# Kernel optimization log

Hardware: AMD Instinct MI355X
Metric: run time of the kernel (lower is better)

Reference implementation:

```python
import jax, jax.numpy as jnp
import numpy as np

B, IN_CH, HID, OUT_CH, GH, GW = 16, 64, 128, 64, 64, 64


def grid_edges(h, w):
    # torch_geometric.utils.grid: 8-neighborhood + self-loop, edge = (node, node+offset)
    idx = np.arange(h * w).reshape(h, w)
    rows, cols = [], []
    for dr in (-1, 0, 1):
        for dc in (-1, 0, 1):
            node = idx[max(0, -dr):h - max(0, dr), max(0, -dc):w - max(0, dc)]
            nb = idx[max(0, dr):h + min(0, dr) or None, max(0, dc):w + min(0, dc) or None]
            rows.append(node.ravel())
            cols.append(nb.ravel())
    return np.stack([np.concatenate(rows), np.concatenate(cols)])


def setup_inputs() -> dict:
    key = jax.random.key(0)
    ks = jax.random.split(key, 32)
    def rn(i, shape, scale=0.05):
        return jax.random.normal(ks[i], shape, dtype=jnp.float32) * scale
    e = grid_edges(GH, GW)                                   # (2, E)
    offs = (np.arange(B) * (GH * GW)).reshape(B, 1, 1)
    ei = (e[None] + offs).transpose(1, 0, 2).reshape(2, -1)  # (2, B*E) batched offsets
    return {
        "x": rn(0, (B, IN_CH, GH, GW), 1.0),
        "cW1": rn(1, (HID, IN_CH, 3, 3)), "cb1": rn(2, (HID,)),
        "cW2": rn(3, (IN_CH, HID, 3, 3)), "cb2": rn(4, (IN_CH,)),
        "q1W": rn(5, (HID, IN_CH)), "q1b": rn(6, (HID,)),
        "k1W": rn(7, (HID, IN_CH)), "k1b": rn(8, (HID,)),
        "v1W": rn(9, (HID, IN_CH)), "v1b": rn(10, (HID,)),
        "s1W": rn(11, (HID, IN_CH)), "s1b": rn(12, (HID,)),
        "q2W": rn(13, (IN_CH, HID)), "q2b": rn(14, (IN_CH,)),
        "k2W": rn(15, (IN_CH, HID)), "k2b": rn(16, (IN_CH,)),
        "v2W": rn(17, (IN_CH, HID)), "v2b": rn(18, (IN_CH,)),
        "s2W": rn(19, (IN_CH, HID)), "s2b": rn(20, (IN_CH,)),
        "fW1": rn(21, (HID, 2 * IN_CH, 3, 3)), "fb1": rn(22, (HID,)),
        "fW2": rn(23, (OUT_CH, HID, 3, 3)), "fb2": rn(24, (OUT_CH,)),
        "edge_index": jnp.asarray(ei, dtype=jnp.int32),
    }


def gelu(x):
    return jax.nn.gelu(x, approximate=False)


def sn_conv(x, W, b):
    # spectral_norm: power iteration on (O, I*k*k) matrix; u,v detached, grad through sigma
    O = W.shape[0]
    Wm = W.reshape(O, -1)
    u = jnp.ones((O,), W.dtype) / jnp.sqrt(jnp.asarray(O, W.dtype))
    for _ in range(3):
        v = Wm.T @ u
        v = v / (jnp.linalg.norm(v) + 1e-12)
        u = Wm @ v
        u = u / (jnp.linalg.norm(u) + 1e-12)
    u = jax.lax.stop_gradient(u)
    v = jax.lax.stop_gradient(v)
    sigma = u @ (Wm @ v)
    Wn = W / sigma
    xp = jnp.pad(x, ((0, 0), (0, 0), (1, 1), (1, 1)), mode='edge')  # replicate padding
    y = jax.lax.conv_general_dilated(xp, Wn, (1, 1), 'VALID',
                                     dimension_numbers=('NCHW', 'OIHW', 'NCHW'))
    return y + b[None, :, None, None]


def tconv(x, src, dst, N, heads, qW, qb, kW, kb, vW, vb, sW, sb):
    # PyG TransformerConv (concat=True, root_weight=True, no edge features)
    d = qW.shape[0] // heads
    q = (x @ qW.T + qb)[dst].reshape(-1, heads, d)
    k = (x @ kW.T + kb)[src].reshape(-1, heads, d)
    v = (x @ vW.T + vb)[src].reshape(-1, heads, d)
    alpha = (q * k).sum(-1) / jnp.sqrt(jnp.asarray(d, x.dtype))      # (E, heads)
    m = jax.ops.segment_max(alpha, dst, num_segments=N)               # scatter-softmax
    a = jnp.exp(alpha - m[dst])
    s = jax.ops.segment_sum(a, dst, num_segments=N)
    a = a / (s[dst] + 1e-16)
    out = jax.ops.segment_sum(a[:, :, None] * v, dst, num_segments=N)  # (N, heads, d)
    return out.reshape(N, heads * d) + x @ sW.T + sb


def reference(x, cW1, cb1, cW2, cb2, q1W, q1b, k1W, k1b, v1W, v1b, s1W, s1b,
              q2W, q2b, k2W, k2b, v2W, v2b, s2W, s2b, fW1, fb1, fW2, fb2, edge_index):
    Bb, C, Hc, Wc = x.shape
    N = Bb * Hc * Wc
    # CNN branch (DoubleConvBlock)
    x1 = gelu(sn_conv(gelu(sn_conv(x, cW1, cb1)), cW2, cb2))
    # GCN branch
    xf = x.transpose(0, 2, 3, 1).reshape(N, C)
    src, dst = edge_index[0], edge_index[1]
    h = gelu(tconv(xf, src, dst, N, 8, q1W, q1b, k1W, k1b, v1W, v1b, s1W, s1b))
    h = gelu(tconv(h, src, dst, N, 1, q2W, q2b, k2W, k2b, v2W, v2b, s2W, s2b))
    x2 = h.reshape(Bb, Hc, Wc, -1).transpose(0, 3, 1, 2)
    # Fusion
    xc = jnp.concatenate([x1, x2], axis=1)
    return gelu(sn_conv(gelu(sn_conv(xc, fW1, fb1)), fW2, fb2))
```

## Files before the change

### kernel.cpp

```cpp
#include <hip/hip_runtime.h>
#include <hip/hip_bf16.h>

typedef unsigned int  u32;
typedef unsigned short u16;
typedef __attribute__((ext_vector_type(8))) short bf16x8;
typedef __attribute__((ext_vector_type(4))) float f32x4;
typedef __attribute__((ext_vector_type(4))) u32 u32x4;

#define NPIX 65536

constexpr size_t SIG   = 0;
constexpr size_t B1OFF = 256;
constexpr size_t B2OFF = B1OFF + 2048;
constexpr size_t WC1   = B2OFF + 1024;
constexpr size_t WC2   = WC1 + 147456;
constexpr size_t WF1   = WC2 + 147456;
constexpr size_t WF2   = WF1 + 294912;
constexpr size_t WP1   = WF2 + 147456;
constexpr size_t WP2   = WP1 + 65536;
constexpr size_t XB    = WP2 + 65536;
constexpr size_t HBUF  = XB + 8388608;
constexpr size_t QKVS2 = HBUF + 16777216;
constexpr size_t XC    = QKVS2 + 33554432;
constexpr size_t QKVS1 = XC + 16777216;
constexpr size_t Y1    = QKVS1;
constexpr size_t TBUF  = QKVS1 + 16777216;
constexpr size_t GRAM  = QKVS1 + 67108864;

__device__ __forceinline__ float gelu_f(float v) {
    float xa = fabsf(v) * 0.70710678118654752f;
    float t  = __fdividef(1.0f, fmaf(0.3275911f, xa, 1.0f));
    float poly = t * fmaf(t, fmaf(t, fmaf(t, fmaf(t, 1.061405429f, -1.453152027f),
                   1.421413741f), -0.284496736f), 0.254829592f);
    float erfv = 1.0f - poly * __expf(-xa * xa);
    erfv = copysignf(erfv, v);
    return 0.5f * v * (1.0f + erfv);
}
__device__ __forceinline__ u16 f2bf(float f) {
    __hip_bfloat16 b = __float2bfloat16(f);
    return *reinterpret_cast<u16*>(&b);
}
__device__ __forceinline__ float blo(u32 u) {
    union { u32 i; float f; } x; x.i = u << 16; return x.f;
}
__device__ __forceinline__ float bhi(u32 u) {
    union { u32 i; float f; } x; x.i = u & 0xffff0000u; return x.f;
}
__device__ __forceinline__ u32 packbf(float a, float b) {
    return (u32)f2bf(a) | ((u32)f2bf(b) << 16);
}
__device__ __forceinline__ void g2l16(const void* g, void* l) {
    __builtin_amdgcn_global_load_lds(
        (const __attribute__((address_space(1))) u32*)g,
        (__attribute__((address_space(3))) u32*)l, 16, 0, 0);
}
template<int N>
__device__ __forceinline__ void waitvm() {
    asm volatile("s_waitcnt vmcnt(%0)" :: "n"(N) : "memory");
}

__device__ float block_sum(float vv, float* red) {
    #pragma unroll
    for (int m = 1; m < 64; m <<= 1) vv += __shfl_xor(vv, m);
    int tid = threadIdx.x;
    __syncthreads();
    if ((tid & 63) == 0) red[tid >> 6] = vv;
    __syncthreads();
    return red[0] + red[1] + red[2] + red[3];
}

__global__ __launch_bounds__(256)
void gram_kernel(const float* __restrict__ cW1, const float* __restrict__ cW2,
                 const float* __restrict__ fW1, const float* __restrict__ fW2,
                 float* __restrict__ Gall) {
    int bid = blockIdx.x;
    const float* W; int O, K, wsel, tile;
    if (bid < 64)       { W = cW1; O = 128; K = 576;  wsel = 0; tile = bid; }
    else if (bid < 80)  { W = cW2; O = 64;  K = 1152; wsel = 1; tile = bid - 64; }
    else if (bid < 144) { W = fW1; O = 128; K = 1152; wsel = 2; tile = bid - 80; }
    else                { W = fW2; O = 64;  K = 1152; wsel = 3; tile = bid - 144; }
    int ntiles = O >> 4;
    int ti0 = (tile / ntiles) << 4, tj0 = (tile % ntiles) << 4;
    __shared__ float Wi[16][33], Wj[16][33];
    int tid = threadIdx.x;
    int ti = tid >> 4, tj = tid & 15;
    int r = tid >> 5, c = tid & 31;
    float acc = 0.f;
    for (int k0 = 0; k0 < K; k0 += 32) {
        Wi[r][c]     = W[(size_t)(ti0 + r) * K + k0 + c];
        Wi[r + 8][c] = W[(size_t)(ti0 + r + 8) * K + k0 + c];
        Wj[r][c]     = W[(size_t)(tj0 + r) * K + k0 + c];
        Wj[r + 8][c] = W[(size_t)(tj0 + r + 8) * K + k0 + c];
        __syncthreads();
        #pragma unroll
        for (int k = 0; k < 32; ++k)
            acc += Wi[ti][k] * Wj[tj][k];
        __syncthreads();
    }
    Gall[wsel * 16384 + (ti0 + ti) * 128 + (tj0 + tj)] = acc;
}

__global__ __launch_bounds__(256)
void power_kernel(const float* __restrict__ Gall, float* __restrict__ sig) {
    int wsel = blockIdx.x;
    const float* G = Gall + wsel * 16384;
    const int O = (wsel == 0 || wsel == 2) ? 128 : 64;
    __shared__ float u[128], t[128], red[4];
    int tid = threadIdx.x;
    if (tid < O) u[tid] = 1.0f / sqrtf((float)O);
    __syncthreads();
    for (int it = 0; it < 3; ++it) {
        if (tid < O) {
            float s = 0.f;
            const float4* gr = reinterpret_cast<const float4*>(G + (size_t)tid * 128);
            for (int j = 0; j < O / 4; ++j) {
                float4 g = gr[j];
                s += g.x * u[4*j] + g.y * u[4*j+1] + g.z * u[4*j+2] + g.w * u[4*j+3];
            }
            t[tid] = s;
        }
        __syncthreads();
        float loc = (tid < O) ? t[tid] * t[tid] : 0.f;
        float nt = sqrtf(block_sum(loc, red));
        if (it == 2) {
            float locd = (tid < O) ? u[tid] * t[tid] : 0.f;
            float dot = block_sum(locd, red);
            if (tid == 0) sig[wsel] = nt / sqrtf(dot + 1e-24f);
        } else {
            if (tid < O) u[tid] = t[tid] / (nt + 1e-12f);
            __syncthreads();
        }
    }
}

__global__ __launch_bounds__(256)
void prep_conv_w(const float* __restrict__ cW1, const float* __restrict__ cW2,
                 const float* __restrict__ fW1, const float* __restrict__ fW2,
                 const float* __restrict__ sig,
                 u16* wc1, u16* wc2, u16* wf1, u16* wf2) {
    int wsel = blockIdx.y;
    const float* src; u16* dst; int O, C;
    switch (wsel) {
        case 0:  src = cW1; dst = wc1; O = 128; C = 64;  break;
        case 1:  src = cW2; dst = wc2; O = 64;  C = 128; break;
        case 2:  src = fW1; dst = wf1; O = 128; C = 128; break;
        default: src = fW2; dst = wf2; O = 64;  C = 128; break;
    }
    int idx = blockIdx.x * 256 + threadIdx.x;
    if (idx >= O * C * 9) return;
    int o = idx / (C * 9);
    int rem = idx - o * (C * 9);
    int ci = rem / 9, tap = rem - ci * 9;
    float v = src[idx] / sig[wsel];
    dst[(size_t)o * (C * 9) + tap * C + ci] = f2bf(v);
}

__global__ __launch_bounds__(256)
void prep_proj(const float* q1W, const float* k1W, const float* v1W, const float* s1W,
               const float* q2W, const float* k2W, const float* v2W, const float* s2W,
               const float* q1b, const float* k1b, const float* v1b, const float* s1b,
               const float* q2b, const float* k2b, const float* v2b, const float* s2b,
               u16* wp1, u16* wp2, float* b1, float* b2) {
    const float* W1[4] = {q1W, k1W, v1W, s1W};
    const float* W2[4] = {q2W, k2W, v2W, s2W};
    const float* Bb1[4] = {q1b, k1b, v1b, s1b};
    const float* Bb2[4] = {q2b, k2b, v2b, s2b};
    int idx = blockIdx.x * 256 + threadIdx.x;
    if (idx < 32768) {
        int w = idx >> 13, r = idx & 8191;
        wp1[(size_t)w * 8192 + r] = f2bf(W1[w][r]);
    } else if (idx < 65536) {
        int j = idx - 32768; int w = j >> 13, r = j & 8191;
        wp2[(size_t)w * 8192 + r] = f2bf(W2[w][r]);
    } else if (idx < 66048) {
        int j = idx - 65536; int w = j >> 7; b1[j] = Bb1[w][j & 127];
    } else if (idx < 66304) {
        int j = idx - 66048; int w = j >> 6; b2[j] = Bb2[w][j & 63];
    }
}

__global__ __launch_bounds__(256)
void convert_x(const float* __restrict__ x, u16* __restrict__ xb) {
    __shared__ float tile[64][65];
    int b = blockIdx.x >> 6, y = blockIdx.x & 63;
    int tid = threadIdx.x;
    #pragma unroll
    for (int i = 0; i < 16; ++i) {
        int c = (tid >> 6) + i * 4;
        tile[c][tid & 63] = x[(((size_t)b * 64 + c) << 12) + (y << 6) + (tid & 63)];
    }
    __syncthreads();
    #pragma unroll
    for (int i = 0; i < 16; ++i) {
        int idx = tid + i * 256;
        int p = idx >> 6, c = idx & 63;
        xb[(((size_t)b << 12) + (y << 6) + p) * 64 + c] = f2bf(tile[c][p]);
    }
}

template<int TAPS, int CC, int BN, int OUTM>
__global__ __launch_bounds__(256)
void mm_kernel(const u16* __restrict__ A, const u16* __restrict__ Bw,
               const float* __restrict__ bias, void* __restrict__ Cout,
               int ostride, int ocol0, int do_gelu) {
    constexpr int K = CC * TAPS;
    constexpr int NSTEP = K / 32;
    constexpr int NF = BN / 32;
    constexpr int HN = BN / 2;
    constexpr int LPS = 1 + BN / 64;
    __shared__ u16 Als[3][64 * 32];
    __shared__ u16 Bls[3][BN * 32];
    const int tid = threadIdx.x;
    const int w = tid >> 6;
    const int lane = tid & 63;
    const int m0 = blockIdx.x * 64;
    const int nt0 = blockIdx.y * BN;
    const int wm = w >> 1, wn = w & 1;
    const int csrc = (((tid & 3) ^ ((tid >> 3) & 3)) << 3);

    const int arow = tid >> 2;
    const int mA = m0 + arow;
    const int yA = (mA >> 6) & 63, xA = mA & 63, ibA = mA & ~4095;
    const u16* Brow0 = Bw + (size_t)(nt0 + arow) * K + csrc;
    const u16* Brow1 = Bw + (size_t)(nt0 + arow + (BN > 64 ? 64 : 0)) * K + csrc;

    int offA[2], offB[NF];
    #pragma unroll
    for (int mf = 0; mf < 2; ++mf) {
        int R = wm * 32 + mf * 16 + (lane & 15);
        int C = ((lane >> 4) ^ ((R >> 1) & 3)) << 3;
        offA[mf] = R * 32 + C;
    }
    #pragma unroll
    for (int nf = 0; nf < NF; ++nf) {
        int Rb = wn * HN + nf * 16 + (lane & 15);
        int Cb = ((lane >> 4) ^ ((Rb >> 1) & 3)) << 3;
        offB[nf] = Rb * 32 + Cb;
    }

    f32x4 acc[2][NF];
    #pragma unroll
    for (int i = 0; i < 2; ++i)
        #pragma unroll
        for (int j = 0; j < NF; ++j) {
            f32x4 z = {0.f, 0.f, 0.f, 0.f};
            acc[i][j] = z;
        }

    auto stage = [&](int s) {
        const int buf = s % 3;
        const int kk = s * 32;
        const u16* ga;
        if constexpr (TAPS == 9) {
            const int tap = kk / CC;
            const int ci0 = kk - tap * CC;
            const int t3 = (tap * 11) >> 5;
            const int dy = t3 - 1, dx = tap - t3 * 3 - 1;
            int yy = min(max(yA + dy, 0), 63), xx = min(max(xA + dx, 0), 63);
            ga = A + (size_t)(ibA | (yy << 6) | xx) * CC + ci0 + csrc;
        } else {
            ga = A + (size_t)mA * CC + kk + csrc;
        }
        g2l16(ga, &Als[buf][w * 512]);
        g2l16(Brow0 + kk, &Bls[buf][w * 512]);
        if constexpr (BN > 64)
            g2l16(Brow1 + kk, &Bls[buf][w * 512 + 2048]);
    };

    stage(0);
    stage(1);

    for (int kt = 0; kt < NSTEP; ++kt) {
        if (kt < NSTEP - 1) waitvm<LPS>(); else waitvm<0>();
        __builtin_amdgcn_s_barrier();
        __builtin_amdgcn_sched_barrier(0);
        if (kt + 2 < NSTEP) stage(kt + 2);
        __builtin_amdgcn_sched_barrier(0);
        const u16* Ab = &Als[kt % 3][0];
        const u16* Bb = &Bls[kt % 3][0];
        bf16x8 af[2];
        #pragma unroll
        for (int mf = 0; mf < 2; ++mf)
            af[mf] = *reinterpret_cast<const bf16x8*>(Ab + offA[mf]);
        #pragma unroll
        for (int nf = 0; nf < NF; ++nf) {
            bf16x8 bfv = *reinterpret_cast<const bf16x8*>(Bb + offB[nf]);
            #pragma unroll
            for (int mf = 0; mf < 2; ++mf)
                acc[mf][nf] = __builtin_amdgcn_mfma_f32_16x16x32_bf16(
                    af[mf], bfv, acc[mf][nf], 0, 0, 0);
        }
    }

    #pragma unroll
    for (int mf = 0; mf < 2; ++mf) {
        int mrow = m0 + wm * 32 + mf * 16 + (lane >> 4) * 4;
        #pragma unroll
        for (int nf = 0; nf < NF; ++nf) {
            int col = nt0 + wn * HN + nf * 16 + (lane & 15);
            float bv = bias[col];
            if (OUTM == 0) {
                u16* Co = (u16*)Cout;
                #pragma unroll
                for (int j = 0; j < 4; ++j) {
                    float v = acc[mf][nf][j] + bv;
                    if (do_gelu) v = gelu_f(v);
                    Co[(size_t)(mrow + j) * ostride + ocol0 + col] = f2bf(v);
                }
            } else {
                float* Co = (float*)Cout;
                int b = m0 >> 12;
                int pixb = (mrow & 4095);
                f32x4 vv;
                #pragma unroll
                for (int j = 0; j < 4; ++j) {
                    float v = acc[mf][nf][j] + bv;
                    vv[j] = gelu_f(v);
                }
                *reinterpret_cast<f32x4*>(&Co[((size_t)(b * 64 + col)) * 4096 + pixb]) = vv;
            }
        }
    }
}

__global__ __launch_bounds__(256)
void attn1_kernel(const u16* __restrict__ qkvs, u16* __restrict__ h) {
    const int tid = threadIdx.x;
    const int l16 = tid & 15;
    const int n = blockIdx.x * 16 + (tid >> 4);
    const int y = (n >> 6) & 63, x = n & 63;
    const u32* qk = (const u32*)qkvs;
    const int nbase = (n << 8) + l16 * 4;

    u32x4 qp = *(const u32x4*)(qk + nbase);
    float q[8];
    #pragma unroll
    for (int i = 0; i < 4; ++i) { q[2*i] = blo(qp[i]); q[2*i+1] = bhi(qp[i]); }

    float al[9];
    float mx = -1e30f;
    #pragma unroll
    for (int e = 0; e < 9; ++e) {
        const int dy = e / 3 - 1, dx = e % 3 - 1;
        const bool valid = (unsigned)(y + dy) < 64u && (unsigned)(x + dx) < 64u;
        const int off = valid ? ((dy * 64 + dx) << 8) : 0;
        u32x4 kp = *(const u32x4*)(qk + nbase + off + 64);
        float p = 0.f;
        #pragma unroll
        for (int i = 0; i < 4; ++i) {
            p = fmaf(q[2*i],   blo(kp[i]), p);
            p = fmaf(q[2*i+1], bhi(kp[i]), p);
        }
        p += __shfl_xor(p, 1);
        al[e] = valid ? p * 0.25f : -1e30f;
        mx = fmaxf(mx, al[e]);
    }
    float s = 0.f;
    #pragma unroll
    for (int e = 0; e < 9; ++e) { al[e] = __expf(al[e] - mx); s += al[e]; }

    float o[8] = {0.f, 0.f, 0.f, 0.f, 0.f, 0.f, 0.f, 0.f};
    #pragma unroll
    for (int e = 0; e < 9; ++e) {
        const int dy = e / 3 - 1, dx = e % 3 - 1;
        const bool valid = (unsigned)(y + dy) < 64u && (unsigned)(x + dx) < 64u;
        const int off = valid ? ((dy * 64 + dx) << 8) : 0;
        u32x4 vp = *(const u32x4*)(qk + nbase + off + 128);
        const float a = al[e];
        #pragma unroll
        for (int i = 0; i < 4; ++i) {
            o[2*i]   = fmaf(a, blo(vp[i]), o[2*i]);
            o[2*i+1] = fmaf(a, bhi(vp[i]), o[2*i+1]);
        }
    }
    const float r = __fdividef(1.0f, s + 1e-16f);
    u32x4 sp = *(const u32x4*)(qk + nbase + 192);
    u32x4 res;
    #pragma unroll
    for (int i = 0; i < 4; ++i) {
        float h0 = gelu_f(fmaf(o[2*i],   r, blo(sp[i])));
        float h1 = gelu_f(fmaf(o[2*i+1], r, bhi(sp[i])));
        res[i] = packbf(h0, h1);
    }
    *(u32x4*)((u32*)h + (n << 6) + l16 * 4) = res;
}

__global__ __launch_bounds__(256)
void attn2_kernel(const u16* __restrict__ qkvs, u16* __restrict__ xc) {
    const int tid = threadIdx.x;
    const int l8 = tid & 7;
    const int n = blockIdx.x * 32 + (tid >> 3);
    const int y = (n >> 6) & 63, x = n & 63;
    const u32* qk = (const u32*)qkvs;
    const int nbase = (n << 7) + l8 * 4;

    u32x4 qp = *(const u32x4*)(qk + nbase);
    float q[8];
    #pragma unroll
    for (int i = 0; i < 4; ++i) { q[2*i] = blo(qp[i]); q[2*i+1] = bhi(qp[i]); }

    float al[9];
    float mx = -1e30f;
    #pragma unroll
    for (int e = 0; e < 9; ++e) {
        const int dy = e / 3 - 1, dx = e % 3 - 1;
        const bool valid = (unsigned)(y + dy) < 64u && (unsigned)(x + dx) < 64u;
        const int off = valid ? ((dy * 64 + dx) << 7) : 0;
        u32x4 kp = *(const u32x4*)(qk + nbase + off + 32);
        float p = 0.f;
        #pragma unroll
        for (int i = 0; i < 4; ++i) {
            p = fmaf(q[2*i],   blo(kp[i]), p);
            p = fmaf(q[2*i+1], bhi(kp[i]), p);
        }
        p += __shfl_xor(p, 1);
        p += __shfl_xor(p, 2);
        p += __shfl_xor(p, 4);
        al[e] = valid ? p * 0.125f : -1e30f;
        mx = fmaxf(mx, al[e]);
    }
    float s = 0.f;
    #pragma unroll
    for (int e = 0; e < 9; ++e) { al[e] = __expf(al[e] - mx); s += al[e]; }

    float o[8] = {0.f, 0.f, 0.f, 0.f, 0.f, 0.f, 0.f, 0.f};
    #pragma unroll
    for (int e = 0; e < 9; ++e) {
        const int dy = e / 3 - 1, dx = e % 3 - 1;
        const bool valid = (unsigned)(y + dy) < 64u && (unsigned)(x + dx) < 64u;
        const int off = valid ? ((dy * 64 + dx) << 7) : 0;
        u32x4 vp = *(const u32x4*)(qk + nbase + off + 64);
        const float a = al[e];
        #pragma unroll
        for (int i = 0; i < 4; ++i) {
            o[2*i]   = fmaf(a, blo(vp[i]), o[2*i]);
            o[2*i+1] = fmaf(a, bhi(vp[i]), o[2*i+1]);
        }
    }
    const float r = __fdividef(1.0f, s + 1e-16f);
    u32x4 sp = *(const u32x4*)(qk + nbase + 96);
    u32x4 res;
    #pragma unroll
    for (int i = 0; i < 4; ++i) {
        float h0 = gelu_f(fmaf(o[2*i],   r, blo(sp[i])));
        float h1 = gelu_f(fmaf(o[2*i+1], r, bhi(sp[i])));
        res[i] = packbf(h0, h1);
    }
    *(u32x4*)((u32*)xc + (n << 6) + 32 + l8 * 4) = res;
}

extern "C" void kernel_launch(void* const* d_in, const int* in_sizes, int n_in,
                              void* d_out, int out_size, void* d_ws, size_t ws_size,
                              hipStream_t stream) {
    const float* x   = (const float*)d_in[0];
    const float* cW1 = (const float*)d_in[1];
    const float* cb1 = (const float*)d_in[2];
    const float* cW2 = (const float*)d_in[3];
    const float* cb2 = (const float*)d_in[4];
    const float* q1W = (const float*)d_in[5];
    const float* q1b = (const float*)d_in[6];
    const float* k1W = (const float*)d_in[7];
    const float* k1b = (const float*)d_in[8];
    const float* v1W = (const float*)d_in[9];
    const float* v1b = (const float*)d_in[10];
    const float* s1W = (const float*)d_in[11];
    const float* s1b = (const float*)d_in[12];
    const float* q2W = (const float*)d_in[13];
    const float* q2b = (const float*)d_in[14];
    const float* k2W = (const float*)d_in[15];
    const float* k2b = (const float*)d_in[16];
    const float* v2W = (const float*)d_in[17];
    const float* v2b = (const float*)d_in[18];
    const float* s2W = (const float*)d_in[19];
    const float* s2b = (const float*)d_in[20];
    const float* fW1 = (const float*)d_in[21];
    const float* fb1 = (const float*)d_in[22];
    const float* fW2 = (const float*)d_in[23];
    const float* fb2 = (const float*)d_in[24];

    char* ws = (char*)d_ws;
    float* sig  = (float*)(ws + SIG);
    float* b1   = (float*)(ws + B1OFF);
    float* b2   = (float*)(ws + B2OFF);
    u16* wc1    = (u16*)(ws + WC1);
    u16* wc2    = (u16*)(ws + WC2);
    u16* wf1    = (u16*)(ws + WF1);
    u16* wf2    = (u16*)(ws + WF2);
    u16* wp1    = (u16*)(ws + WP1);
    u16* wp2    = (u16*)(ws + WP2);
    u16* xb     = (u16*)(ws + XB);
    u16* hbuf   = (u16*)(ws + HBUF);
    u16* qkvs2  = (u16*)(ws + QKVS2);
    u16* xc     = (u16*)(ws + XC);
    u16* qkvs1  = (u16*)(ws + QKVS1);
    u16* y1     = (u16*)(ws + Y1);
    u16* tbuf   = (u16*)(ws + TBUF);
    float* gram = (float*)(ws + GRAM);
    float* out  = (float*)d_out;

    gram_kernel<<<160, 256, 0, stream>>>(cW1, cW2, fW1, fW2, gram);
    power_kernel<<<4, 256, 0, stream>>>(gram, sig);
    prep_conv_w<<<dim3(576, 4), 256, 0, stream>>>(cW1, cW2, fW1, fW2, sig,
                                                  wc1, wc2, wf1, wf2);
    prep_proj<<<260, 256, 0, stream>>>(q1W, k1W, v1W, s1W, q2W, k2W, v2W, s2W,
                                       q1b, k1b, v1b, s1b, q2b, k2b, v2b, s2b,
                                       wp1, wp2, b1, b2);
    convert_x<<<1024, 256, 0, stream>>>(x, xb);

    mm_kernel<1, 64, 128, 0><<<dim3(1024, 4), 256, 0, stream>>>(
        xb, wp1, b1, qkvs1, 512, 0, 0);
    attn1_kernel<<<NPIX / 16, 256, 0, stream>>>(qkvs1, hbuf);
    mm_kernel<1, 128, 128, 0><<<dim3(1024, 2), 256, 0, stream>>>(
        hbuf, wp2, b2, qkvs2, 256, 0, 0);
    attn2_kernel<<<NPIX / 32, 256, 0, stream>>>(qkvs2, xc);

    mm_kernel<9, 64, 128, 0><<<dim3(1024, 1), 256, 0, stream>>>(
        xb, wc1, cb1, y1, 128, 0, 1);
    mm_kernel<9, 128, 64, 0><<<dim3(1024, 1), 256, 0, stream>>>(
        y1, wc2, cb2, xc, 128, 0, 1);
    mm_kernel<9, 128, 128, 0><<<dim3(1024, 1), 256, 0, stream>>>(
        xc, wf1, fb1, tbuf, 128, 0, 1);
    mm_kernel<9, 128, 64, 1><<<dim3(1024, 1), 256, 0, stream>>>(
        tbuf, wf2, fb2, out, 0, 0, 1);
}
```

Measured before the change: 232.2 us.

## Double the GEMM K-tile to 64 with an 8-way swizzled LDS layout

Result: slower. 246.4 us (+6.1%).

```diff
diff --git a/kernel.cpp b/kernel.cpp
--- a/kernel.cpp
+++ b/kernel.cpp
@@ -204,38 +204,42 @@
                const float* __restrict__ bias, void* __restrict__ Cout,
                int ostride, int ocol0, int do_gelu) {
     constexpr int K = CC * TAPS;
-    constexpr int NSTEP = K / 32;
+    constexpr int NSTEP = K / 64;
     constexpr int NF = BN / 32;
     constexpr int HN = BN / 2;
-    constexpr int LPS = 1 + BN / 64;
-    __shared__ u16 Als[3][64 * 32];
-    __shared__ u16 Bls[3][BN * 32];
+    constexpr int LPS = 2 + BN / 32;
+    __shared__ u16 Als[3][64 * 64];
+    __shared__ u16 Bls[3][BN * 64];
     const int tid = threadIdx.x;
     const int w = tid >> 6;
     const int lane = tid & 63;
     const int m0 = blockIdx.x * 64;
     const int nt0 = blockIdx.y * BN;
     const int wm = w >> 1, wn = w & 1;
-    const int csrc = (((tid & 3) ^ ((tid >> 3) & 3)) << 3);
-
-    const int arow = tid >> 2;
-    const int mA = m0 + arow;
-    const int yA = (mA >> 6) & 63, xA = mA & 63, ibA = mA & ~4095;
-    const u16* Brow0 = Bw + (size_t)(nt0 + arow) * K + csrc;
-    const u16* Brow1 = Bw + (size_t)(nt0 + arow + (BN > 64 ? 64 : 0)) * K + csrc;
-
-    int offA[2], offB[NF];
-    #pragma unroll
-    for (int mf = 0; mf < 2; ++mf) {
-        int R = wm * 32 + mf * 16 + (lane & 15);
-        int C = ((lane >> 4) ^ ((R >> 1) & 3)) << 3;
-        offA[mf] = R * 32 + C;
-    }
-    #pragma unroll
-    for (int nf = 0; nf < NF; ++nf) {
-        int Rb = wn * HN + nf * 16 + (lane & 15);
-        int Cb = ((lane >> 4) ^ ((Rb >> 1) & 3)) << 3;
-        offB[nf] = Rb * 32 + Cb;
+    const int cg8 = (((tid & 7) ^ ((tid >> 3) & 7)) << 3);
+
+    const int r0 = (w << 3) + ((tid >> 3) & 7);
+    const int mA0 = m0 + r0;
+    const int mA1 = mA0 + 32;
+    const int yA = (mA0 >> 6) & 63, ibA = mA0 & ~4095;
+    const int xA0 = mA0 & 63, xA1 = mA1 & 63;
+    const u16* Bbase = Bw + (size_t)(nt0 + r0) * K + cg8;
+
+    int offA[2][2], offB[2][NF];
+    #pragma unroll
+    for (int s = 0; s < 2; ++s) {
+        #pragma unroll
+        for (int mf = 0; mf < 2; ++mf) {
+            int R = wm * 32 + mf * 16 + (lane & 15);
+            int cl = s * 4 + (lane >> 4);
+            offA[s][mf] = R * 64 + ((cl ^ (R & 7)) << 3);
+        }
+        #pragma unroll
+        for (int nf = 0; nf < NF; ++nf) {
+            int Rb = wn * HN + nf * 16 + (lane & 15);
+            int cl = s * 4 + (lane >> 4);
+            offB[s][nf] = Rb * 64 + ((cl ^ (Rb & 7)) << 3);
+        }
     }
 
     f32x4 acc[2][NF];
@@ -249,26 +253,31 @@
 
     auto stage = [&](int s) {
         const int buf = s % 3;
-        const int kk = s * 32;
-        const u16* ga;
+        const int kk = s * 64;
+        const u16 *ga0, *ga1;
         if constexpr (TAPS == 9) {
             const int tap = kk / CC;
             const int ci0 = kk - tap * CC;
             const int t3 = (tap * 11) >> 5;
             const int dy = t3 - 1, dx = tap - t3 * 3 - 1;
-            int yy = min(max(yA + dy, 0), 63), xx = min(max(xA + dx, 0), 63);
-            ga = A + (size_t)(ibA | (yy << 6) | xx) * CC + ci0 + csrc;
+            const int yy = min(max(yA + dy, 0), 63);
+            const int xx0 = min(max(xA0 + dx, 0), 63);
+            const int xx1 = min(max(xA1 + dx, 0), 63);
+            ga0 = A + (size_t)(ibA | (yy << 6) | xx0) * CC + ci0 + cg8;
+            ga1 = A + (size_t)(ibA | (yy << 6) | xx1) * CC + ci0 + cg8;
         } else {
-            ga = A + (size_t)mA * CC + kk + csrc;
-        }
-        g2l16(ga, &Als[buf][w * 512]);
-        g2l16(Brow0 + kk, &Bls[buf][w * 512]);
-        if constexpr (BN > 64)
-            g2l16(Brow1 + kk, &Bls[buf][w * 512 + 2048]);
+            ga0 = A + (size_t)mA0 * CC + kk + cg8;
+            ga1 = A + (size_t)mA1 * CC + kk + cg8;
+        }
+        g2l16(ga0, &Als[buf][(w << 3) * 64]);
+        g2l16(ga1, &Als[buf][(32 + (w << 3)) * 64]);
+        #pragma unroll
+        for (int i = 0; i < BN / 32; ++i)
+            g2l16(Bbase + (size_t)i * 32 * K + kk, &Bls[buf][(i * 32 + (w << 3)) * 64]);
     };
 
     stage(0);
-    stage(1);
+    if constexpr (NSTEP > 1) stage(1);
 
     for (int kt = 0; kt < NSTEP; ++kt) {
         if (kt < NSTEP - 1) waitvm<LPS>(); else waitvm<0>();
@@ -278,17 +287,20 @@
         __builtin_amdgcn_sched_barrier(0);
         const u16* Ab = &Als[kt % 3][0];
         const u16* Bb = &Bls[kt % 3][0];
-        bf16x8 af[2];
-        #pragma unroll
-        for (int mf = 0; mf < 2; ++mf)
-            af[mf] = *reinterpret_cast<const bf16x8*>(Ab + offA[mf]);
-        #pragma unroll
-        for (int nf = 0; nf < NF; ++nf) {
-            bf16x8 bfv = *reinterpret_cast<const bf16x8*>(Bb + offB[nf]);
+        #pragma unroll
+        for (int s = 0; s < 2; ++s) {
+            bf16x8 af[2];
             #pragma unroll
             for (int mf = 0; mf < 2; ++mf)
-                acc[mf][nf] = __builtin_amdgcn_mfma_f32_16x16x32_bf16(
-                    af[mf], bfv, acc[mf][nf], 0, 0, 0);
+                af[mf] = *reinterpret_cast<const bf16x8*>(Ab + offA[s][mf]);
+            #pragma unroll
+            for (int nf = 0; nf < NF; ++nf) {
+                bf16x8 bfv = *reinterpret_cast<const bf16x8*>(Bb + offB[s][nf]);
+                #pragma unroll
+                for (int mf = 0; mf < 2; ++mf)
+                    acc[mf][nf] = __builtin_amdgcn_mfma_f32_16x16x32_bf16(
+                        af[mf], bfv, acc[mf][nf], 0, 0, 0);
+            }
         }
     }
 
```
